# Performance work log

Hardware: AMD Instinct MI355X
Metric: run time of the kernel (lower is better)

## Reference

```python
import jax, jax.numpy as jnp
import numpy as np

# DAttentionBaseline config (matches init_kwargs)
NH, HC, G = 8, 32, 4          # n_heads, n_head_channels, n_groups
ORF = 2.0                      # offset_range_factor
KK = 5                         # offset conv kernel (stage_idx=2)


def _conv1x1(x, w, b=None):
    # x: (B,C,H,W), w: (O,C)
    y = jnp.einsum('bchw,oc->bohw', x, w)
    return y if b is None else y + b[None, :, None, None]


def _ref_points(Hk, Wk, dtype):
    # replicates torch.meshgrid(..., indexing='xy') as in the source
    ly = jnp.linspace(0.5, Hk - 0.5, Hk, dtype=dtype)
    lx = jnp.linspace(0.5, Wk - 0.5, Wk, dtype=dtype)
    ry, rx = jnp.meshgrid(ly, lx, indexing='xy')  # shapes (Wk, Hk); Hk==Wk here
    return jnp.stack([ry / Hk * 2 - 1, rx / Wk * 2 - 1], axis=-1)  # (Hk,Wk,2)


def _grid_sample(img, grid):
    # bilinear, align_corners=True, zero padding. img:(N,C,Hi,Wi), grid:(N,Hg,Wg,2) in [-1,1] (x,y)
    N, C, Hi, Wi = img.shape
    gx = (grid[..., 0] + 1.0) * 0.5 * (Wi - 1)
    gy = (grid[..., 1] + 1.0) * 0.5 * (Hi - 1)
    x0 = jnp.floor(gx); y0 = jnp.floor(gy)
    x1 = x0 + 1.0;      y1 = y0 + 1.0
    wx1 = gx - x0; wx0 = 1.0 - wx1
    wy1 = gy - y0; wy0 = 1.0 - wy1
    nidx = jnp.arange(N)[:, None, None]

    def gather(yf, xf):
        valid = (xf >= 0) & (xf <= Wi - 1) & (yf >= 0) & (yf <= Hi - 1)
        xi = jnp.clip(xf, 0, Wi - 1).astype(jnp.int32)
        yi = jnp.clip(yf, 0, Hi - 1).astype(jnp.int32)
        vals = img[nidx, :, yi, xi]  # (N,Hg,Wg,C)
        return vals * valid[..., None].astype(img.dtype)

    out = (gather(y0, x0) * (wy0 * wx0)[..., None]
           + gather(y0, x1) * (wy0 * wx1)[..., None]
           + gather(y1, x0) * (wy1 * wx0)[..., None]
           + gather(y1, x1) * (wy1 * wx1)[..., None])
    return out.transpose(0, 3, 1, 2)  # (N,C,Hg,Wg)


def _forward(x, wq, bq, w_off_dw, b_off_dw, ln_g, ln_b, w_off_pj, wk, bk, wv, bv, wo, bo, rpe_table):
    B, C, H, W = x.shape
    GC = C // G            # group channels
    GH = NH // G           # group heads
    scale = HC ** -0.5

    q = _conv1x1(x, wq, bq)                                   # (B,C,H,W)
    q_off = q.reshape(B * G, GC, H, W)

    # conv_offset: depthwise conv -> LayerNorm over channels -> GELU -> 1x1 conv to 2
    off = jax.lax.conv_general_dilated(
        q_off, w_off_dw, (1, 1), [(KK // 2, KK // 2), (KK // 2, KK // 2)],
        feature_group_count=GC, dimension_numbers=('NCHW', 'OIHW', 'NCHW'))
    off = off + b_off_dw[None, :, None, None]
    mu = off.mean(axis=1, keepdims=True)
    var = off.var(axis=1, keepdims=True)
    off = (off - mu) * jax.lax.rsqrt(var + 1e-5)
    off = off * ln_g[None, :, None, None] + ln_b[None, :, None, None]
    off = jax.nn.gelu(off, approximate=False)
    offset = jnp.einsum('bchw,oc->bohw', off, w_off_pj)       # (B*G,2,Hk,Wk)

    Hk, Wk = offset.shape[2], offset.shape[3]
    ns = Hk * Wk
    rng = jnp.array([1.0 / Hk, 1.0 / Wk], dtype=x.dtype).reshape(1, 2, 1, 1)
    offset = jnp.tanh(offset) * rng * ORF                     # offset_range_factor > 0
    offset = offset.transpose(0, 2, 3, 1)                     # (B*G,Hk,Wk,2)

    ref = _ref_points(Hk, Wk, x.dtype)                        # (Hk,Wk,2)
    pos = offset + ref[None]                                  # (B*G,Hk,Wk,2), (y,x) order

    xs = _grid_sample(x.reshape(B * G, GC, H, W), pos[..., ::-1])  # (B*G,GC,Hk,Wk)
    xs = xs.reshape(B, C, 1, ns)

    k = _conv1x1(xs, wk, bk).reshape(B * NH, HC, ns)
    v = _conv1x1(xs, wv, bv).reshape(B * NH, HC, ns)
    qf = q.reshape(B * NH, HC, H * W)
    attn = jnp.einsum('bcm,bcn->bmn', qf, k) * scale          # (B*NH, HW, ns)

    # RPE via grid_sample on the (2H-1, 2W-1) bias table
    rpe = jnp.broadcast_to(rpe_table[None], (B,) + rpe_table.shape)
    rpe = rpe.reshape(B * G, GH, 2 * H - 1, 2 * W - 1)
    qg = _ref_points(H, W, x.dtype).reshape(H * W, 2)
    disp = (qg[None, :, None, :] - pos.reshape(B * G, ns, 2)[:, None, :, :]) * 0.5  # (B*G,HW,ns,2)
    bias = _grid_sample(rpe, disp[..., ::-1]).reshape(B * NH, H * W, ns)
    attn = attn + bias

    attn = jax.nn.softmax(attn, axis=2)
    out = jnp.einsum('bmn,bcn->bcm', attn, v).reshape(B, C, H, W)
    y = _conv1x1(out, wo, bo)
    return (y,
            pos.reshape(B, G, Hk, Wk, 2),
            jnp.broadcast_to(ref[None, None], (B, G, Hk, Wk, 2)))


def setup_inputs() -> dict:
    key = jax.random.key(0)
    ks = jax.random.split(key, 8)
    B, C, H, W = 4, 256, 32, 32
    GC = C // G
    s = 0.02

    def n(k, shape, sc=s):
        return jax.random.normal(k, shape, jnp.float32) * sc

    return {
        'x': jax.random.normal(ks[0], (B, C, H, W), jnp.float32),
        'wq': n(ks[1], (C, C)), 'bq': jnp.zeros((C,), jnp.float32),
        'w_off_dw': n(ks[2], (GC, 1, KK, KK)), 'b_off_dw': jnp.zeros((GC,), jnp.float32),
        'ln_g': jnp.ones((GC,), jnp.float32), 'ln_b': jnp.zeros((GC,), jnp.float32),
        'w_off_pj': n(ks[3], (2, GC)),
        'wk': n(ks[4], (C, C)), 'bk': jnp.zeros((C,), jnp.float32),
        'wv': n(ks[5], (C, C)), 'bv': jnp.zeros((C,), jnp.float32),
        'wo': n(ks[6], (C, C)), 'bo': jnp.zeros((C,), jnp.float32),
        'rpe_table': n(ks[7], (NH, 2 * H - 1, 2 * W - 1), 0.01),
    }


def reference(x, wq, bq, w_off_dw, b_off_dw, ln_g, ln_b, w_off_pj, wk, bk, wv, bv, wo, bo, rpe_table):
    return _forward(x, wq, bq, w_off_dw, b_off_dw, ln_g, ln_b, w_off_pj, wk, bk, wv, bv, wo, bo, rpe_table)
```

## Files before the change

kernel.cpp:

```cpp
#include <hip/hip_runtime.h>
#include <math.h>

#define CK __restrict__

constexpr int CH = 256;
constexpr int HW = 1024;

typedef __attribute__((ext_vector_type(8))) short short8;
typedef __attribute__((ext_vector_type(4))) float f32x4;
typedef __attribute__((ext_vector_type(2))) float v2f;

__device__ __forceinline__ ushort f2b(float x) {
    union { float f; unsigned int u; } a; a.f = x;
    unsigned int r = (a.u + 0x7FFFu + ((a.u >> 16) & 1u)) >> 16;
    return (ushort)r;
}
__device__ __forceinline__ short8 ld8(const ushort* p) { return *(const short8*)p; }
__device__ __forceinline__ float u2f(unsigned int u) {
    union { unsigned int u; float f; } a; a.u = u; return a.f;
}
__device__ __forceinline__ float b2f(ushort us) { return u2f((unsigned int)us << 16); }

__global__ __launch_bounds__(256) void prep(const float* CK w0, const float* CK w1,
                                            const float* CK w2, const float* CK w3,
                                            ushort* CK o0, ushort* CK o1,
                                            ushort* CK o2, ushort* CK o3,
                                            const float* CK x, ushort* CK xT,
                                            const float* CK rpe, unsigned int* CK rpetab) {
    const int bid = blockIdx.x, t = threadIdx.x;
    if (bid < 256) {
        const float* src; ushort* dst;
        switch (bid >> 6) {
            case 0: src = w0; dst = o0; break;
            case 1: src = w1; dst = o1; break;
            case 2: src = w2; dst = o2; break;
            default: src = w3; dst = o3; break;
        }
        const int i = (bid & 63) * 256 + t;
        float4 v = ((const float4*)src)[i];
        ushort4 r; r.x = f2b(v.x); r.y = f2b(v.y); r.z = f2b(v.z); r.w = f2b(v.w);
        ((ushort4*)dst)[i] = r;
    } else if (bid < 384) {
        const int b2 = bid - 256;
        const int c8 = b2 & 31, b = b2 >> 5;
        for (int nn = 0; nn < 4; nn++) {
            const int n = nn * 256 + t;
            union { ushort u[8]; short8 s; } pk;
#pragma unroll
            for (int j = 0; j < 8; j++) pk.u[j] = f2b(x[(b * 256 + c8 * 8 + j) * HW + n]);
            *(short8*)(xT + b * 262144 + n * 256 + c8 * 8) = pk.s;
        }
    } else {
        const int h = bid - 384;
        const float* rp = rpe + h * 3969;
        unsigned int* dst = rpetab + h * 4356;
        for (int i = t; i < 4356; i += 256) {
            int y = i / 67, x2 = i - y * 67;
            int yy = y - 1, xx = x2 - 1;
            bool vy = (yy >= 0) && (yy < 63) && (y < 65);
            float a  = (vy && xx >= 0 && xx < 63) ? rp[yy * 63 + xx] : 0.f;
            float bb = (vy && xx >= -1 && xx < 62) ? rp[yy * 63 + xx + 1] : 0.f;
            dst[i] = (unsigned int)f2b(a) | ((unsigned int)f2b(bb) << 16);
        }
    }
}

__global__ __launch_bounds__(256) void gemm_q(const ushort* CK AT, const ushort* CK W,
                                              const float* CK bias, ushort* CK Y) {
    const int b = blockIdx.z;
    const int t = threadIdx.x, w = t >> 6, l = t & 63;
    const int lm = l & 15, qd = l >> 4;
    const int m0 = blockIdx.y * 64 + (w & 1) * 32;
    const int n0 = blockIdx.x * 64 + (w >> 1) * 32;
    const ushort* A = AT + b * 262144 + n0 * 256;
    const ushort* Bm = W + m0 * 256;
    f32x4 acc[2][2] = {};
#pragma unroll
    for (int k0 = 0; k0 < 8; k0++) {
        const int ko = k0 * 32 + qd * 8;
        short8 a0 = ld8(A + lm * 256 + ko);
        short8 a1 = ld8(A + (16 + lm) * 256 + ko);
        short8 b0 = ld8(Bm + lm * 256 + ko);
        short8 b1 = ld8(Bm + (16 + lm) * 256 + ko);
        acc[0][0] = __builtin_amdgcn_mfma_f32_16x16x32_bf16(a0, b0, acc[0][0], 0, 0, 0);
        acc[0][1] = __builtin_amdgcn_mfma_f32_16x16x32_bf16(a0, b1, acc[0][1], 0, 0, 0);
        acc[1][0] = __builtin_amdgcn_mfma_f32_16x16x32_bf16(a1, b0, acc[1][0], 0, 0, 0);
        acc[1][1] = __builtin_amdgcn_mfma_f32_16x16x32_bf16(a1, b1, acc[1][1], 0, 0, 0);
    }
#pragma unroll
    for (int in = 0; in < 2; in++)
#pragma unroll
        for (int im = 0; im < 2; im++) {
            const int m = m0 + im * 16 + lm;
            const float bs = bias[m];
            ushort4 r;
            r.x = f2b(acc[in][im][0] + bs); r.y = f2b(acc[in][im][1] + bs);
            r.z = f2b(acc[in][im][2] + bs); r.w = f2b(acc[in][im][3] + bs);
            *(ushort4*)(Y + b * 262144 + m * HW + n0 + in * 16 + qd * 4) = r;
        }
}

__global__ __launch_bounds__(256) void gemm_kv(const ushort* CK AT,
                                               const ushort* CK Wk, const float* CK bk, ushort* CK kbt,
                                               const ushort* CK Wv, const float* CK bv, ushort* CK vbs) {
    const int b = blockIdx.z;
    const int t = threadIdx.x, w = t >> 6, l = t & 63;
    const int lm = l & 15, qd = l >> 4;
    const int m0 = blockIdx.y * 64 + (w & 1) * 32;
    const int n0 = blockIdx.x * 64 + (w >> 1) * 32;
    const ushort* A = AT + b * 262144 + n0 * 256;
    const ushort* Bk = Wk + m0 * 256;
    const ushort* Bv = Wv + m0 * 256;
    f32x4 akT[2][2] = {}, av[2][2] = {};
#pragma unroll
    for (int k0 = 0; k0 < 8; k0++) {
        const int ko = k0 * 32 + qd * 8;
        short8 a0 = ld8(A + lm * 256 + ko);
        short8 a1 = ld8(A + (16 + lm) * 256 + ko);
        short8 k0f = ld8(Bk + lm * 256 + ko);
        short8 k1f = ld8(Bk + (16 + lm) * 256 + ko);
        short8 v0f = ld8(Bv + lm * 256 + ko);
        short8 v1f = ld8(Bv + (16 + lm) * 256 + ko);
        akT[0][0] = __builtin_amdgcn_mfma_f32_16x16x32_bf16(k0f, a0, akT[0][0], 0, 0, 0);
        akT[0][1] = __builtin_amdgcn_mfma_f32_16x16x32_bf16(k0f, a1, akT[0][1], 0, 0, 0);
        akT[1][0] = __builtin_amdgcn_mfma_f32_16x16x32_bf16(k1f, a0, akT[1][0], 0, 0, 0);
        akT[1][1] = __builtin_amdgcn_mfma_f32_16x16x32_bf16(k1f, a1, akT[1][1], 0, 0, 0);
        av[0][0] = __builtin_amdgcn_mfma_f32_16x16x32_bf16(a0, v0f, av[0][0], 0, 0, 0);
        av[0][1] = __builtin_amdgcn_mfma_f32_16x16x32_bf16(a0, v1f, av[0][1], 0, 0, 0);
        av[1][0] = __builtin_amdgcn_mfma_f32_16x16x32_bf16(a1, v0f, av[1][0], 0, 0, 0);
        av[1][1] = __builtin_amdgcn_mfma_f32_16x16x32_bf16(a1, v1f, av[1][1], 0, 0, 0);
    }
#pragma unroll
    for (int im = 0; im < 2; im++)
#pragma unroll
        for (int in = 0; in < 2; in++) {
            {
                const int c0 = m0 + im * 16 + qd * 4;
                const int n  = n0 + in * 16 + lm;
                const int bh = b * 8 + (c0 >> 5);
                const int qdk = (c0 & 31) >> 3, co4 = c0 & 7;
                const int nc = n >> 7, nbk = (n >> 4) & 7, lmk = n & 15;
                const float4 bks = *(const float4*)(bk + c0);
                ushort4 r4;
                r4.x = f2b(akT[im][in][0] + bks.x);
                r4.y = f2b(akT[im][in][1] + bks.y);
                r4.z = f2b(akT[im][in][2] + bks.z);
                r4.w = f2b(akT[im][in][3] + bks.w);
                *(ushort4*)(kbt + ((bh * 8 + nc) * 512 + nbk * 64 + qdk * 16 + lmk) * 8 + co4) = r4;
            }
            {
                const int c = m0 + im * 16 + lm;
                const int bh = b * 8 + (c >> 5);
                const float bs = bv[c];
                const int cb = (c & 31) >> 4, lmv = c & 15;
                const int nbase = n0 + in * 16 + qd * 4;
                const int nc = nbase >> 7, kc = (nbase >> 5) & 3;
                const int qdv = (nbase >> 3) & 3, co0 = nbase & 7;
                ushort4 r4;
                r4.x = f2b(av[in][im][0] + bs); r4.y = f2b(av[in][im][1] + bs);
                r4.z = f2b(av[in][im][2] + bs); r4.w = f2b(av[in][im][3] + bs);
                *(ushort4*)(vbs + ((bh * 8 + nc) * 512 + (cb * 4 + kc) * 64 + qdv * 16 + lmv) * 8 + co0) = r4;
            }
        }
}

__global__ __launch_bounds__(256) void dwconv(const ushort* CK q, const float* CK wdw,
                                              const float* CK bdw, float* CK off) {
    const int bx = blockIdx.x;
    const int ch = bx & 63;
    const ushort* qb = q + bx * HW;
    float w[25];
#pragma unroll
    for (int i = 0; i < 25; i++) w[i] = wdw[ch * 25 + i];
    const float bb = bdw[ch];
    const int t = threadIdx.x;
#pragma unroll
    for (int p = 0; p < 4; p++) {
        int hw = p * 256 + t;
        int ii = hw >> 5, jj = hw & 31;
        float s = bb;
#pragma unroll
        for (int ky = 0; ky < 5; ky++) {
            int y = ii + ky - 2;
            if (y < 0 || y > 31) continue;
#pragma unroll
            for (int kx = 0; kx < 5; kx++) {
                int x = jj + kx - 2;
                if (x < 0 || x > 31) continue;
                s += b2f(qb[y * 32 + x]) * w[ky * 5 + kx];
            }
        }
        off[bx * HW + hw] = s;
    }
}

__global__ __launch_bounds__(256) void lnps(const float* CK off, const float* CK ln_g,
                                            const float* CK ln_b, const float* CK wpj,
                                            const float* CK x,
                                            float* CK out_pos, float* CK out_ref,
                                            float2* CK pos_sc, ushort* CK xsT) {
    const int bid = blockIdx.x, t = threadIdx.x;
    const int bg = bid >> 4;
    const int pix_l = t >> 2, qtr = t & 3;
    const int n = (bid & 15) * 64 + pix_l;
    const int gid = bg * 1024 + n;
    const float* ob = off + bg * 64 * HW + n;
    const int c0 = qtr * 16;
    float v[16];
    float s1 = 0.f;
#pragma unroll
    for (int j = 0; j < 16; j++) { v[j] = ob[(c0 + j) * HW]; s1 += v[j]; }
    s1 += __shfl_xor(s1, 1); s1 += __shfl_xor(s1, 2);
    const float mean = s1 * 0.015625f;
    float s2 = 0.f;
#pragma unroll
    for (int j = 0; j < 16; j++) { float d = v[j] - mean; s2 += d * d; }
    s2 += __shfl_xor(s2, 1); s2 += __shfl_xor(s2, 2);
    const float rs = rsqrtf(s2 * 0.015625f + 1e-5f);
    float p0 = 0.f, p1 = 0.f;
#pragma unroll
    for (int j = 0; j < 16; j++) {
        float vv = (v[j] - mean) * rs * ln_g[c0 + j] + ln_b[c0 + j];
        float gl = 0.5f * vv * (1.f + erff(vv * 0.70710678118654752f));
        p0 += gl * wpj[c0 + j];
        p1 += gl * wpj[64 + c0 + j];
    }
    p0 += __shfl_xor(p0, 1); p0 += __shfl_xor(p0, 2);
    p1 += __shfl_xor(p1, 1); p1 += __shfl_xor(p1, 2);
    const int ii = n >> 5, jj = n & 31;
    const float r0 = (jj + 0.5f) * 0.0625f - 1.f;
    const float r1 = (ii + 0.5f) * 0.0625f - 1.f;
    const float pos0 = tanhf(p0) * 0.0625f + r0;
    const float pos1 = tanhf(p1) * 0.0625f + r1;
    if (qtr == 0) {
        out_pos[gid * 2] = pos0; out_pos[gid * 2 + 1] = pos1;
        out_ref[gid * 2] = r0;   out_ref[gid * 2 + 1] = r1;
        pos_sc[gid].x = pos0 * 15.5f; pos_sc[gid].y = pos1 * 15.5f;
    }
    const float gx = (pos1 + 1.f) * 15.5f, gy = (pos0 + 1.f) * 15.5f;
    const float x0f = floorf(gx), y0f = floorf(gy);
    const float wx1 = gx - x0f, wx0 = 1.f - wx1, wy1 = gy - y0f, wy0 = 1.f - wy1;
    const bool vx0 = (x0f >= 0.f) && (x0f <= 31.f);
    const bool vx1 = (x0f >= -1.f) && (x0f <= 30.f);
    const bool vy0 = (y0f >= 0.f) && (y0f <= 31.f);
    const bool vy1 = (y0f >= -1.f) && (y0f <= 30.f);
    const int xi0 = (int)fminf(fmaxf(x0f, 0.f), 31.f);
    const int xi1 = (int)fminf(fmaxf(x0f + 1.f, 0.f), 31.f);
    const int yi0 = (int)fminf(fmaxf(y0f, 0.f), 31.f);
    const int yi1 = (int)fminf(fmaxf(y0f + 1.f, 0.f), 31.f);
    const float w00 = (vy0 && vx0) ? wy0 * wx0 : 0.f;
    const float w01 = (vy0 && vx1) ? wy0 * wx1 : 0.f;
    const float w10 = (vy1 && vx0) ? wy1 * wx0 : 0.f;
    const float w11 = (vy1 && vx1) ? wy1 * wx1 : 0.f;
    const int o00 = yi0 * 32 + xi0, o01 = yi0 * 32 + xi1;
    const int o10 = yi1 * 32 + xi0, o11 = yi1 * 32 + xi1;
    const int b = bg >> 2, g = bg & 3;
    const float* xb = x + bg * 64 * HW;
    ushort* xo = xsT + b * 262144 + n * 256 + g * 64 + c0;
#pragma unroll
    for (int j4 = 0; j4 < 4; j4++) {
        ushort4 r4;
        float vals[4];
#pragma unroll
        for (int j = 0; j < 4; j++) {
            const float* p = xb + (c0 + j4 * 4 + j) * HW;
            vals[j] = w00 * p[o00] + w01 * p[o01] + w10 * p[o10] + w11 * p[o11];
        }
        r4.x = f2b(vals[0]); r4.y = f2b(vals[1]); r4.z = f2b(vals[2]); r4.w = f2b(vals[3]);
        *(ushort4*)(xo + j4 * 4) = r4;
    }
}

__global__ __launch_bounds__(256, 4) void attn_part(const ushort* CK q, const ushort* CK kbt,
                                                    const ushort* CK vbs, const float2* CK pos_sc,
                                                    const unsigned int* CK rpetab,
                                                    ushort* CK partO, float2* CK mlbuf) {
    __shared__ __align__(16) unsigned int rpe_pr[4356];
    __shared__ __align__(16) ushort Pl[4][1088];
    const int bh = blockIdx.y, quarter = blockIdx.z;
    const int b = bh >> 3, nh = bh & 7, bg = bh >> 1;
    const int t = threadIdx.x;
    const int w = t >> 6, l = t & 63;
    const int lm = l & 15, qd = l >> 4;

    {
        const uint4* src4 = (const uint4*)(rpetab + nh * 4356);
        uint4* dst4 = (uint4*)rpe_pr;
        for (int i = t; i < 1089; i += 256) dst4[i] = src4[i];
    }
    __syncthreads();

    const int m = blockIdx.x * 64 + w * 16 + lm;
    short8 qf;
    {
        union { ushort u[8]; short8 s; } pk;
        const ushort* qb = q + (b * 256 + nh * 32) * HW + m;
#pragma unroll
        for (int j = 0; j < 8; j++) pk.u[j] = qb[(qd * 8 + j) * HW];
        qf = pk.s;
    }
    const float qg0 = ((m & 31) + 0.5f) * 0.0625f - 1.f;
    const float qg1 = ((m >> 5) + 0.5f) * 0.0625f - 1.f;
    const float ax = 31.f + 15.5f * qg1;
    const float ay = 31.f + 15.5f * qg0;

    f32x4 oacc0 = {0.f, 0.f, 0.f, 0.f}, oacc1 = {0.f, 0.f, 0.f, 0.f};
    float rmax = -3e38f, rsum = 0.f;
    ushort* PlW = Pl[w];
    const float2* pbase = pos_sc + bg * 1024;

    for (int nc = quarter * 2; nc < quarter * 2 + 2; nc++) {
        const ushort* kg = kbt + (bh * 8 + nc) * 4096;
        const ushort* vg = vbs + (bh * 8 + nc) * 4096;

#pragma unroll
        for (int g = 0; g < 2; g++) {
            f32x4 sT[4];
#pragma unroll
            for (int s = 0; s < 4; s++) {
                const int nb = g * 4 + s;
                sT[s] = __builtin_amdgcn_mfma_f32_16x16x32_bf16(
                            ld8(kg + (nb * 64 + l) * 8), qf,
                            (f32x4){0.f, 0.f, 0.f, 0.f}, 0, 0, 0);
            }
            float cmax = -3e38f;
#pragma unroll
            for (int s = 0; s < 4; s++) {
                const float4* pp = (const float4*)(pbase + nc * 128 + (g * 4 + s) * 16 + qd * 4);
                const float4 pa = pp[0], pb_ = pp[1];
                const float psx[4] = {pa.x, pa.z, pb_.x, pb_.z};
                const float psy[4] = {pa.y, pa.w, pb_.y, pb_.w};
#pragma unroll
                for (int rp = 0; rp < 2; rp++) {
                    v2f gx = {ax - psy[rp * 2], ax - psy[rp * 2 + 1]};
                    v2f gy = {ay - psx[rp * 2], ay - psx[rp * 2 + 1]};
                    const int xi0 = (int)gx.x, xi1 = (int)gx.y;
                    const int yi0 = (int)gy.x, yi1 = (int)gy.y;
                    v2f wx = gx - (v2f){(float)xi0, (float)xi1};
                    v2f wy = gy - (v2f){(float)yi0, (float)yi1};
                    const int idxA = yi0 * 67 + xi0 + 68;
                    const int idxB = yi1 * 67 + xi1 + 68;
                    const unsigned int a0 = rpe_pr[idxA], a1 = rpe_pr[idxA + 67];
                    const unsigned int b0 = rpe_pr[idxB], b1 = rpe_pr[idxB + 67];
                    v2f tA = {u2f(a0 << 16), u2f(a0 & 0xFFFF0000u)};
                    v2f bA = {u2f(a1 << 16), u2f(a1 & 0xFFFF0000u)};
                    v2f tB = {u2f(b0 << 16), u2f(b0 & 0xFFFF0000u)};
                    v2f bB = {u2f(b1 << 16), u2f(b1 & 0xFFFF0000u)};
                    v2f vA = tA + wy.x * (bA - tA);
                    v2f vB = tB + wy.y * (bB - tB);
                    const float biasA = vA.x + wx.x * (vA.y - vA.x);
                    const float biasB = vB.x + wx.y * (vB.y - vB.x);
                    sT[s][rp * 2]     = sT[s][rp * 2]     * 0.17677669529663687f + biasA;
                    sT[s][rp * 2 + 1] = sT[s][rp * 2 + 1] * 0.17677669529663687f + biasB;
                    cmax = fmaxf(cmax, fmaxf(sT[s][rp * 2], sT[s][rp * 2 + 1]));
                }
            }
            cmax = fmaxf(cmax, __shfl_xor(cmax, 16));
            cmax = fmaxf(cmax, __shfl_xor(cmax, 32));
            const float newmax = fmaxf(rmax, cmax);
            const float alpha = __expf(rmax - newmax);
            rmax = newmax;
            float csum = 0.f;
#pragma unroll
            for (int s = 0; s < 4; s++) {
                float e0 = __expf(sT[s][0] - rmax);
                float e1 = __expf(sT[s][1] - rmax);
                float e2 = __expf(sT[s][2] - rmax);
                float e3 = __expf(sT[s][3] - rmax);
                csum += (e0 + e1) + (e2 + e3);
                uint2 pk;
                pk.x = (unsigned int)f2b(e0) | ((unsigned int)f2b(e1) << 16);
                pk.y = (unsigned int)f2b(e2) | ((unsigned int)f2b(e3) << 16);
                *(uint2*)(PlW + s * 272 + l * 4) = pk;
            }
            csum += __shfl_xor(csum, 16);
            csum += __shfl_xor(csum, 32);
            rsum = rsum * alpha + csum;
            oacc0 *= alpha;
            oacc1 *= alpha;
#pragma unroll
            for (int kc = 0; kc < 2; kc++) {
                const ushort* pb2 = PlW + (kc * 2 + (qd >> 1)) * 272 + (qd & 1) * 128 + lm * 4;
                union { uint2 u[2]; short8 s; } pfu;
                pfu.u[0] = *(const uint2*)pb2;
                pfu.u[1] = *(const uint2*)(pb2 + 64);
                const int kv = g * 2 + kc;
                oacc0 = __builtin_amdgcn_mfma_f32_16x16x32_bf16(ld8(vg + (kv * 64 + l) * 8), pfu.s, oacc0, 0, 0, 0);
                oacc1 = __builtin_amdgcn_mfma_f32_16x16x32_bf16(ld8(vg + ((4 + kv) * 64 + l) * 8), pfu.s, oacc1, 0, 0, 0);
            }
        }
    }

    ushort* po = partO + (((quarter * 32 + bh) * 1024 + m) * 32) + qd * 4;
    ushort4 r04, r14;
    r04.x = f2b(oacc0[0]); r04.y = f2b(oacc0[1]); r04.z = f2b(oacc0[2]); r04.w = f2b(oacc0[3]);
    r14.x = f2b(oacc1[0]); r14.y = f2b(oacc1[1]); r14.z = f2b(oacc1[2]); r14.w = f2b(oacc1[3]);
    *(ushort4*)po = r04;
    *(ushort4*)(po + 16) = r14;
    if (qd == 0) {
        float2 ml; ml.x = rmax; ml.y = rsum;
        mlbuf[(quarter * 32 + bh) * 1024 + m] = ml;
    }
}

__global__ __launch_bounds__(256) void gemm_oc(const ushort* CK partO, const float2* CK mlbuf,
                                               const ushort* CK W, const float* CK bias,
                                               float* CK Y) {
    __shared__ __align__(16) float ew[64][8][4];
    const int b = blockIdx.z;
    const int t = threadIdx.x, w = t >> 6, l = t & 63;
    const int lm = l & 15, qd = l >> 4;
    const int m0 = blockIdx.y * 64 + (w & 1) * 32;
    const int n0 = blockIdx.x * 64 + (w >> 1) * 32;
    const int nblk = blockIdx.x * 64;

    for (int p = t; p < 512; p += 256) {
        const int pix = p >> 3, head = p & 7;
        const int mg = nblk + pix;
        const int bh = b * 8 + head;
        float2 ml[4];
        float M = -3e38f;
#pragma unroll
        for (int q2 = 0; q2 < 4; q2++) {
            ml[q2] = mlbuf[(q2 * 32 + bh) * 1024 + mg];
            M = fmaxf(M, ml[q2].x);
        }
        float e[4], den = 0.f;
#pragma unroll
        for (int q2 = 0; q2 < 4; q2++) { e[q2] = __expf(ml[q2].x - M); den += ml[q2].y * e[q2]; }
        const float inv = 1.f / den;
#pragma unroll
        for (int q2 = 0; q2 < 4; q2++) ew[pix][head][q2] = e[q2] * inv;
    }
    __syncthreads();

    const ushort* Bm = W + m0 * 256;
    f32x4 acc[2][2] = {};
#pragma unroll
    for (int k0 = 0; k0 < 8; k0++) {
        const int ko = k0 * 32 + qd * 8;
        short8 af[2];
#pragma unroll
        for (int half = 0; half < 2; half++) {
            const int pix_l = (w >> 1) * 32 + half * 16 + lm;
            const int mg = nblk + pix_l;
            const ushort* pbq = partO + ((b * 8 + k0) * 1024 + mg) * 32 + qd * 8;
            const float4 e4 = *(const float4*)&ew[pix_l][k0][0];
            float a8[8] = {};
#pragma unroll
            for (int q2 = 0; q2 < 4; q2++) {
                union { ushort u[8]; short8 s; } pv;
                pv.s = ld8(pbq + q2 * 1048576);
                const float eq = (q2 == 0) ? e4.x : (q2 == 1) ? e4.y : (q2 == 2) ? e4.z : e4.w;
#pragma unroll
                for (int j = 0; j < 8; j++) a8[j] += b2f(pv.u[j]) * eq;
            }
            union { ushort u[8]; short8 s; } out;
#pragma unroll
            for (int j = 0; j < 8; j++) out.u[j] = f2b(a8[j]);
            af[half] = out.s;
        }
        short8 b0 = ld8(Bm + lm * 256 + ko);
        short8 b1 = ld8(Bm + (16 + lm) * 256 + ko);
        acc[0][0] = __builtin_amdgcn_mfma_f32_16x16x32_bf16(af[0], b0, acc[0][0], 0, 0, 0);
        acc[0][1] = __builtin_amdgcn_mfma_f32_16x16x32_bf16(af[0], b1, acc[0][1], 0, 0, 0);
        acc[1][0] = __builtin_amdgcn_mfma_f32_16x16x32_bf16(af[1], b0, acc[1][0], 0, 0, 0);
        acc[1][1] = __builtin_amdgcn_mfma_f32_16x16x32_bf16(af[1], b1, acc[1][1], 0, 0, 0);
    }
#pragma unroll
    for (int in = 0; in < 2; in++)
#pragma unroll
        for (int im = 0; im < 2; im++) {
            const int mo = m0 + im * 16 + lm;
            const float bs = bias[mo];
            float4 r;
            r.x = acc[in][im][0] + bs; r.y = acc[in][im][1] + bs;
            r.z = acc[in][im][2] + bs; r.w = acc[in][im][3] + bs;
            *(float4*)(Y + b * 262144 + mo * HW + n0 + in * 16 + qd * 4) = r;
        }
}

extern "C" void kernel_launch(void* const* d_in, const int* in_sizes, int n_in,
                              void* d_out, int out_size, void* d_ws, size_t ws_size,
                              hipStream_t stream) {
    (void)in_sizes; (void)n_in; (void)out_size; (void)ws_size;
    const float* x   = (const float*)d_in[0];
    const float* wq  = (const float*)d_in[1];
    const float* bq  = (const float*)d_in[2];
    const float* wdw = (const float*)d_in[3];
    const float* bdw = (const float*)d_in[4];
    const float* lng = (const float*)d_in[5];
    const float* lnb = (const float*)d_in[6];
    const float* wpj = (const float*)d_in[7];
    const float* wk  = (const float*)d_in[8];
    const float* bk  = (const float*)d_in[9];
    const float* wv  = (const float*)d_in[10];
    const float* bv  = (const float*)d_in[11];
    const float* wo  = (const float*)d_in[12];
    const float* bo  = (const float*)d_in[13];
    const float* rpe = (const float*)d_in[14];
    float* outp = (float*)d_out;
    char* base = (char*)d_ws;
    const size_t MB = 1 << 20;

    ushort* q_b    = (ushort*)(base);
    ushort* kbt    = (ushort*)(base + 2 * MB);
    ushort* vbs    = (ushort*)(base + 4 * MB);
    float*  off_ws = (float*)(base + 6 * MB);
    ushort* xT     = (ushort*)(base + 10 * MB);
    ushort* xsT    = (ushort*)(base + 12 * MB);
    ushort* partO  = (ushort*)(base + 6 * MB);
    float2* mlbuf  = (float2*)(base + 14 * MB);
    ushort* wqb    = (ushort*)(base + 15 * MB);
    ushort* wkb    = (ushort*)(base + 15 * MB + 131072);
    ushort* wvb    = (ushort*)(base + 15 * MB + 262144);
    ushort* wob    = (ushort*)(base + 15 * MB + 393216);
    float2* pos_sc = (float2*)(base + 15 * MB + 524288);
    unsigned int* rpetab = (unsigned int*)(base + 15 * MB + 655360);

    prep<<<392, 256, 0, stream>>>(wq, wk, wv, wo, wqb, wkb, wvb, wob, x, xT, rpe, rpetab);
    gemm_q<<<dim3(16, 4, 4), 256, 0, stream>>>(xT, wqb, bq, q_b);
    dwconv<<<1024, 256, 0, stream>>>(q_b, wdw, bdw, off_ws);
    lnps<<<256, 256, 0, stream>>>(off_ws, lng, lnb, wpj, x,
                                  outp + (1 << 20), outp + (1 << 20) + 32768, pos_sc, xsT);
    gemm_kv<<<dim3(16, 4, 4), 256, 0, stream>>>(xsT, wkb, bk, kbt, wvb, bv, vbs);
    attn_part<<<dim3(16, 32, 4), 256, 0, stream>>>(q_b, kbt, vbs, pos_sc, rpetab, partO, mlbuf);
    gemm_oc<<<dim3(16, 4, 4), 256, 0, stream>>>(partO, mlbuf, wob, bo, outp);
}
```

Measured before the change: 182.5 us.

## Drop prep kernel; convert fp32 weights/x to bf16 inside GEMMs, transpose dwconv output

Removes the separate prep pass that converted the four weight matrices and x to bf16. Each GEMM now loads fp32 operands and rounds them to bf16 in registers, and gemm_q reads x directly with strided loads. The rpe table build moves into extra blocks of gemm_q. dwconv now writes its output channel-last, so lnps can read 16 contiguous floats with vector loads. This saves a launch and an intermediate round trip through memory, at the cost of twice the weight traffic per GEMM tile, uncoalesced strided loads of x in gemm_q, and redundant conversion work in every block.

```diff
diff --git a/kernel.cpp b/kernel.cpp
--- a/kernel.cpp
+++ b/kernel.cpp
@@ -21,37 +21,26 @@
 }
 __device__ __forceinline__ float b2f(ushort us) { return u2f((unsigned int)us << 16); }
 
-__global__ __launch_bounds__(256) void prep(const float* CK w0, const float* CK w1,
-                                            const float* CK w2, const float* CK w3,
-                                            ushort* CK o0, ushort* CK o1,
-                                            ushort* CK o2, ushort* CK o3,
-                                            const float* CK x, ushort* CK xT,
-                                            const float* CK rpe, unsigned int* CK rpetab) {
+__device__ __forceinline__ short8 cvt8(const float* CK p) {
+    union { ushort u[8]; short8 s; } r;
+    const float4 v0 = *(const float4*)p, v1 = *(const float4*)(p + 4);
+    r.u[0] = f2b(v0.x); r.u[1] = f2b(v0.y); r.u[2] = f2b(v0.z); r.u[3] = f2b(v0.w);
+    r.u[4] = f2b(v1.x); r.u[5] = f2b(v1.y); r.u[6] = f2b(v1.z); r.u[7] = f2b(v1.w);
+    return r.s;
+}
+__device__ __forceinline__ short8 cvt8s(const float* CK p) {
+    union { ushort u[8]; short8 s; } r;
+#pragma unroll
+    for (int j = 0; j < 8; j++) r.u[j] = f2b(p[j * 1024]);
+    return r.s;
+}
+
+__global__ __launch_bounds__(256) void gemm_q(const float* CK x, const float* CK wq,
+                                              const float* CK bias, ushort* CK Y,
+                                              const float* CK rpe, unsigned int* CK rpetab) {
     const int bid = blockIdx.x, t = threadIdx.x;
-    if (bid < 256) {
-        const float* src; ushort* dst;
-        switch (bid >> 6) {
-            case 0: src = w0; dst = o0; break;
-            case 1: src = w1; dst = o1; break;
-            case 2: src = w2; dst = o2; break;
-            default: src = w3; dst = o3; break;
-        }
-        const int i = (bid & 63) * 256 + t;
-        float4 v = ((const float4*)src)[i];
-        ushort4 r; r.x = f2b(v.x); r.y = f2b(v.y); r.z = f2b(v.z); r.w = f2b(v.w);
-        ((ushort4*)dst)[i] = r;
-    } else if (bid < 384) {
-        const int b2 = bid - 256;
-        const int c8 = b2 & 31, b = b2 >> 5;
-        for (int nn = 0; nn < 4; nn++) {
-            const int n = nn * 256 + t;
-            union { ushort u[8]; short8 s; } pk;
-#pragma unroll
-            for (int j = 0; j < 8; j++) pk.u[j] = f2b(x[(b * 256 + c8 * 8 + j) * HW + n]);
-            *(short8*)(xT + b * 262144 + n * 256 + c8 * 8) = pk.s;
-        }
-    } else {
-        const int h = bid - 384;
+    if (bid >= 256) {
+        const int h = bid - 256;
         const float* rp = rpe + h * 3969;
         unsigned int* dst = rpetab + h * 4356;
         for (int i = t; i < 4356; i += 256) {
@@ -62,26 +51,23 @@
             float bb = (vy && xx >= -1 && xx < 62) ? rp[yy * 63 + xx + 1] : 0.f;
             dst[i] = (unsigned int)f2b(a) | ((unsigned int)f2b(bb) << 16);
         }
-    }
-}
-
-__global__ __launch_bounds__(256) void gemm_q(const ushort* CK AT, const ushort* CK W,
-                                              const float* CK bias, ushort* CK Y) {
-    const int b = blockIdx.z;
-    const int t = threadIdx.x, w = t >> 6, l = t & 63;
+        return;
+    }
+    const int b = bid >> 6, my = (bid >> 4) & 3, nx = bid & 15;
+    const int w = t >> 6, l = t & 63;
     const int lm = l & 15, qd = l >> 4;
-    const int m0 = blockIdx.y * 64 + (w & 1) * 32;
-    const int n0 = blockIdx.x * 64 + (w >> 1) * 32;
-    const ushort* A = AT + b * 262144 + n0 * 256;
-    const ushort* Bm = W + m0 * 256;
+    const int m0 = my * 64 + (w & 1) * 32;
+    const int n0 = nx * 64 + (w >> 1) * 32;
+    const float* A = x + b * 262144 + n0;
+    const float* Bm = wq + m0 * 256;
     f32x4 acc[2][2] = {};
 #pragma unroll
     for (int k0 = 0; k0 < 8; k0++) {
         const int ko = k0 * 32 + qd * 8;
-        short8 a0 = ld8(A + lm * 256 + ko);
-        short8 a1 = ld8(A + (16 + lm) * 256 + ko);
-        short8 b0 = ld8(Bm + lm * 256 + ko);
-        short8 b1 = ld8(Bm + (16 + lm) * 256 + ko);
+        short8 a0 = cvt8s(A + ko * 1024 + lm);
+        short8 a1 = cvt8s(A + ko * 1024 + 16 + lm);
+        short8 b0 = cvt8(Bm + lm * 256 + ko);
+        short8 b1 = cvt8(Bm + (16 + lm) * 256 + ko);
         acc[0][0] = __builtin_amdgcn_mfma_f32_16x16x32_bf16(a0, b0, acc[0][0], 0, 0, 0);
         acc[0][1] = __builtin_amdgcn_mfma_f32_16x16x32_bf16(a0, b1, acc[0][1], 0, 0, 0);
         acc[1][0] = __builtin_amdgcn_mfma_f32_16x16x32_bf16(a1, b0, acc[1][0], 0, 0, 0);
@@ -101,26 +87,26 @@
 }
 
 __global__ __launch_bounds__(256) void gemm_kv(const ushort* CK AT,
-                                               const ushort* CK Wk, const float* CK bk, ushort* CK kbt,
-                                               const ushort* CK Wv, const float* CK bv, ushort* CK vbs) {
+                                               const float* CK Wk, const float* CK bk, ushort* CK kbt,
+                                               const float* CK Wv, const float* CK bv, ushort* CK vbs) {
     const int b = blockIdx.z;
     const int t = threadIdx.x, w = t >> 6, l = t & 63;
     const int lm = l & 15, qd = l >> 4;
     const int m0 = blockIdx.y * 64 + (w & 1) * 32;
     const int n0 = blockIdx.x * 64 + (w >> 1) * 32;
     const ushort* A = AT + b * 262144 + n0 * 256;
-    const ushort* Bk = Wk + m0 * 256;
-    const ushort* Bv = Wv + m0 * 256;
+    const float* Bk = Wk + m0 * 256;
+    const float* Bv = Wv + m0 * 256;
     f32x4 akT[2][2] = {}, av[2][2] = {};
 #pragma unroll
     for (int k0 = 0; k0 < 8; k0++) {
         const int ko = k0 * 32 + qd * 8;
         short8 a0 = ld8(A + lm * 256 + ko);
         short8 a1 = ld8(A + (16 + lm) * 256 + ko);
-        short8 k0f = ld8(Bk + lm * 256 + ko);
-        short8 k1f = ld8(Bk + (16 + lm) * 256 + ko);
-        short8 v0f = ld8(Bv + lm * 256 + ko);
-        short8 v1f = ld8(Bv + (16 + lm) * 256 + ko);
+        short8 k0f = cvt8(Bk + lm * 256 + ko);
+        short8 k1f = cvt8(Bk + (16 + lm) * 256 + ko);
+        short8 v0f = cvt8(Bv + lm * 256 + ko);
+        short8 v1f = cvt8(Bv + (16 + lm) * 256 + ko);
         akT[0][0] = __builtin_amdgcn_mfma_f32_16x16x32_bf16(k0f, a0, akT[0][0], 0, 0, 0);
         akT[0][1] = __builtin_amdgcn_mfma_f32_16x16x32_bf16(k0f, a1, akT[0][1], 0, 0, 0);
         akT[1][0] = __builtin_amdgcn_mfma_f32_16x16x32_bf16(k1f, a0, akT[1][0], 0, 0, 0);
@@ -165,9 +151,9 @@
 }
 
 __global__ __launch_bounds__(256) void dwconv(const ushort* CK q, const float* CK wdw,
-                                              const float* CK bdw, float* CK off) {
+                                              const float* CK bdw, float* CK off_t) {
     const int bx = blockIdx.x;
-    const int ch = bx & 63;
+    const int bg = bx >> 6, ch = bx & 63;
     const ushort* qb = q + bx * HW;
     float w[25];
 #pragma unroll
@@ -190,11 +176,11 @@
                 s += b2f(qb[y * 32 + x]) * w[ky * 5 + kx];
             }
         }
-        off[bx * HW + hw] = s;
-    }
-}
-
-__global__ __launch_bounds__(256) void lnps(const float* CK off, const float* CK ln_g,
+        off_t[bg * 65536 + hw * 64 + ch] = s;
+    }
+}
+
+__global__ __launch_bounds__(256) void lnps(const float* CK off_t, const float* CK ln_g,
                                             const float* CK ln_b, const float* CK wpj,
                                             const float* CK x,
                                             float* CK out_pos, float* CK out_ref,
@@ -204,12 +190,19 @@
     const int pix_l = t >> 2, qtr = t & 3;
     const int n = (bid & 15) * 64 + pix_l;
     const int gid = bg * 1024 + n;
-    const float* ob = off + bg * 64 * HW + n;
     const int c0 = qtr * 16;
     float v[16];
+    {
+        const float4* ov = (const float4*)(off_t + bg * 65536 + n * 64 + c0);
+        const float4 V0 = ov[0], V1 = ov[1], V2 = ov[2], V3 = ov[3];
+        v[0] = V0.x;  v[1] = V0.y;  v[2] = V0.z;  v[3] = V0.w;
+        v[4] = V1.x;  v[5] = V1.y;  v[6] = V1.z;  v[7] = V1.w;
+        v[8] = V2.x;  v[9] = V2.y;  v[10] = V2.z; v[11] = V2.w;
+        v[12] = V3.x; v[13] = V3.y; v[14] = V3.z; v[15] = V3.w;
+    }
     float s1 = 0.f;
 #pragma unroll
-    for (int j = 0; j < 16; j++) { v[j] = ob[(c0 + j) * HW]; s1 += v[j]; }
+    for (int j = 0; j < 16; j++) s1 += v[j];
     s1 += __shfl_xor(s1, 1); s1 += __shfl_xor(s1, 2);
     const float mean = s1 * 0.015625f;
     float s2 = 0.f;
@@ -404,7 +397,7 @@
 }
 
 __global__ __launch_bounds__(256) void gemm_oc(const ushort* CK partO, const float2* CK mlbuf,
-                                               const ushort* CK W, const float* CK bias,
+                                               const float* CK W, const float* CK bias,
                                                float* CK Y) {
     __shared__ __align__(16) float ew[64][8][4];
     const int b = blockIdx.z;
@@ -434,7 +427,7 @@
     }
     __syncthreads();
 
-    const ushort* Bm = W + m0 * 256;
+    const float* Bm = W + m0 * 256;
     f32x4 acc[2][2] = {};
 #pragma unroll
     for (int k0 = 0; k0 < 8; k0++) {
@@ -460,8 +453,8 @@
             for (int j = 0; j < 8; j++) out.u[j] = f2b(a8[j]);
             af[half] = out.s;
         }
-        short8 b0 = ld8(Bm + lm * 256 + ko);
-        short8 b1 = ld8(Bm + (16 + lm) * 256 + ko);
+        short8 b0 = cvt8(Bm + lm * 256 + ko);
+        short8 b1 = cvt8(Bm + (16 + lm) * 256 + ko);
         acc[0][0] = __builtin_amdgcn_mfma_f32_16x16x32_bf16(af[0], b0, acc[0][0], 0, 0, 0);
         acc[0][1] = __builtin_amdgcn_mfma_f32_16x16x32_bf16(af[0], b1, acc[0][1], 0, 0, 0);
         acc[1][0] = __builtin_amdgcn_mfma_f32_16x16x32_bf16(af[1], b0, acc[1][0], 0, 0, 0);
@@ -506,24 +499,18 @@
     ushort* q_b    = (ushort*)(base);
     ushort* kbt    = (ushort*)(base + 2 * MB);
     ushort* vbs    = (ushort*)(base + 4 * MB);
-    float*  off_ws = (float*)(base + 6 * MB);
-    ushort* xT     = (ushort*)(base + 10 * MB);
-    ushort* xsT    = (ushort*)(base + 12 * MB);
+    float*  off_t  = (float*)(base + 6 * MB);
+    ushort* xsT    = (ushort*)(base + 10 * MB);
     ushort* partO  = (ushort*)(base + 6 * MB);
     float2* mlbuf  = (float2*)(base + 14 * MB);
-    ushort* wqb    = (ushort*)(base + 15 * MB);
-    ushort* wkb    = (ushort*)(base + 15 * MB + 131072);
-    ushort* wvb    = (ushort*)(base + 15 * MB + 262144);
-    ushort* wob    = (ushort*)(base + 15 * MB + 393216);
-    float2* pos_sc = (float2*)(base + 15 * MB + 524288);
-    unsigned int* rpetab = (unsigned int*)(base + 15 * MB + 655360);
-
-    prep<<<392, 256, 0, stream>>>(wq, wk, wv, wo, wqb, wkb, wvb, wob, x, xT, rpe, rpetab);
-    gemm_q<<<dim3(16, 4, 4), 256, 0, stream>>>(xT, wqb, bq, q_b);
-    dwconv<<<1024, 256, 0, stream>>>(q_b, wdw, bdw, off_ws);
-    lnps<<<256, 256, 0, stream>>>(off_ws, lng, lnb, wpj, x,
+    float2* pos_sc = (float2*)(base + 15 * MB);
+    unsigned int* rpetab = (unsigned int*)(base + 15 * MB + 131072);
+
+    gemm_q<<<264, 256, 0, stream>>>(x, wq, bq, q_b, rpe, rpetab);
+    dwconv<<<1024, 256, 0, stream>>>(q_b, wdw, bdw, off_t);
+    lnps<<<256, 256, 0, stream>>>(off_t, lng, lnb, wpj, x,
                                   outp + (1 << 20), outp + (1 << 20) + 32768, pos_sc, xsT);
-    gemm_kv<<<dim3(16, 4, 4), 256, 0, stream>>>(xsT, wkb, bk, kbt, wvb, bv, vbs);
+    gemm_kv<<<dim3(16, 4, 4), 256, 0, stream>>>(xsT, wk, bk, kbt, wv, bv, vbs);
     attn_part<<<dim3(16, 32, 4), 256, 0, stream>>>(q_b, kbt, vbs, pos_sc, rpetab, partO, mlbuf);
-    gemm_oc<<<dim3(16, 4, 4), 256, 0, stream>>>(partO, mlbuf, wob, bo, outp);
-}
+    gemm_oc<<<dim3(16, 4, 4), 256, 0, stream>>>(partO, mlbuf, wo, bo, outp);
+}
```

Result: slower. 190.3 us (+4.3%).
